# Performance work log

Measured on AMD Instinct MI355X. Metric: run time of the kernel, lower is better.

## Reference

```python
import jax, jax.numpy as jnp
import numpy as np

B, S, H, NH, T = 128, 512, 768, 8, 20
HD = H // NH


def setup_inputs() -> dict:
    key = jax.random.key(0)
    ks = jax.random.split(key, 16)
    f32 = jnp.float32
    def W(i, *shape):
        return jax.random.normal(ks[i], shape, f32) * 0.02
    inp = {}
    inp["ehs"] = jax.random.normal(ks[0], (B, S, H), f32)
    inp["relevance"] = jax.random.uniform(ks[1], (B, 1), dtype=f32)
    inp["threshold"] = jnp.array([0.5], f32)
    # text_to_caption_proj: Linear, LeakyReLU, LayerNorm, Linear
    inp["tW1"] = W(2, H, H); inp["tb1"] = jnp.zeros((H,), f32)
    inp["tg"] = jnp.ones((H,), f32); inp["tbe"] = jnp.zeros((H,), f32)
    inp["tW2"] = W(3, H, H); inp["tb2"] = jnp.zeros((H,), f32)
    # image_to_caption_proj
    inp["iW1"] = W(4, H, H); inp["ib1"] = jnp.zeros((H,), f32)
    inp["ig"] = jnp.ones((H,), f32); inp["ibe"] = jnp.zeros((H,), f32)
    inp["iW2"] = W(5, H, H); inp["ib2"] = jnp.zeros((H,), f32)
    # nn.MultiheadAttention packed in_proj [3H,H] + out_proj [H,H], x2
    inp["taWin"] = W(6, 3 * H, H); inp["taBin"] = jnp.zeros((3 * H,), f32)
    inp["taWout"] = W(7, H, H); inp["taBout"] = jnp.zeros((H,), f32)
    inp["iaWin"] = W(8, 3 * H, H); inp["iaBin"] = jnp.zeros((3 * H,), f32)
    inp["iaWout"] = W(9, H, H); inp["iaBout"] = jnp.zeros((H,), f32)
    # length_adapter: Linear, LayerNorm, ReLU
    inp["laW"] = W(10, H, H); inp["laB"] = jnp.zeros((H,), f32)
    inp["laG"] = jnp.ones((H,), f32); inp["laBe"] = jnp.zeros((H,), f32)
    # quality_estimator: Linear(H,H/2), LayerNorm, ReLU, Linear(H/2,1), Sigmoid
    inp["qW1"] = W(11, H // 2, H); inp["qB1"] = jnp.zeros((H // 2,), f32)
    inp["qG"] = jnp.ones((H // 2,), f32); inp["qBe"] = jnp.zeros((H // 2,), f32)
    inp["qW2"] = W(12, 1, H // 2); inp["qB2"] = jnp.zeros((1,), f32)
    # masks: first half = text tokens, second half = image tokens; no valid
    # image caption => torch loop gives batch_max_length=0 => target_length=20
    pos = jnp.arange(S)
    inp["sentence_mask"] = jnp.tile((pos < S // 2).astype(jnp.int32)[None], (B, 1))
    inp["image_mask"] = jnp.tile((pos >= S // 2).astype(jnp.int32)[None], (B, 1))
    inp["image_caption_mask"] = jnp.zeros((B, S), jnp.int32)
    inp["image_caption_valid"] = jnp.zeros((B,), jnp.int32)
    return inp


def _ln(x, g, b, eps=1e-5):
    m = x.mean(-1, keepdims=True)
    v = ((x - m) ** 2).mean(-1, keepdims=True)
    return (x - m) / jnp.sqrt(v + eps) * g + b


def _mha(q, k, v, Win, bIn, Wout, bOut, key_pad):
    # torch nn.MultiheadAttention, batch_first=True
    Wq, Wk, Wv = jnp.split(Win, 3, axis=0)
    bq, bk, bv = jnp.split(bIn, 3, axis=0)
    def heads(x, Wp, bp):  # [B,L,H] -> [B,NH,L,HD]
        return (x @ Wp.T + bp).reshape(x.shape[0], x.shape[1], NH, HD).transpose(0, 2, 1, 3)
    qh, kh, vh = heads(q, Wq, bq), heads(k, Wk, bk), heads(v, Wv, bv)
    scores = jnp.einsum('bhqd,bhkd->bhqk', qh, kh) / jnp.sqrt(jnp.float32(HD))
    scores = jnp.where(key_pad[:, None, None, :], -1e9, scores)
    attn = jax.nn.softmax(scores, axis=-1)
    out = jnp.einsum('bhqk,bhkd->bhqd', attn, vh)
    out = out.transpose(0, 2, 1, 3).reshape(q.shape[0], q.shape[1], H)
    return out @ Wout.T + bOut


def _sinusoid_pe():
    # vectorized replacement of the scalar double for-loop
    pos = jnp.arange(T, dtype=jnp.float32)[:, None]            # [T,1]
    i = jnp.arange(0, H, 2, dtype=jnp.float32)                 # [H/2]
    ang = pos / (10000.0 ** (i / H))                           # [T,H/2]
    pe = jnp.zeros((T, H), jnp.float32)
    pe = pe.at[:, 0::2].set(jnp.sin(ang)).at[:, 1::2].set(jnp.cos(ang))
    return pe[None]  # [1,T,H]


def reference(ehs, relevance, threshold,
              tW1, tb1, tg, tbe, tW2, tb2,
              iW1, ib1, ig, ibe, iW2, ib2,
              taWin, taBin, taWout, taBout,
              iaWin, iaBin, iaWout, iaBout,
              laW, laB, laG, laBe,
              qW1, qB1, qG, qBe, qW2, qB2,
              sentence_mask, image_mask, image_caption_mask, image_caption_valid):
    sm = sentence_mask.astype(jnp.float32)[..., None]   # [B,S,1]
    im = image_mask.astype(jnp.float32)[..., None]
    text_emb = ehs * sm
    image_emb = ehs * im
    # image_caption_valid is all False => target_length = min(20, max_length-2) = T (static)
    text_len = jnp.clip(sm.sum(axis=1), 1e-9)            # [B,1]
    img_len = jnp.clip(im.sum(axis=1), 1e-9)
    text_pooled = (text_emb * sm).sum(axis=1) / text_len  # mask applied twice, as in torch
    image_pooled = (image_emb * im).sum(axis=1) / img_len
    def proj(x, W1, b1, g, be, W2, b2):
        h = jax.nn.leaky_relu(x @ W1.T + b1, 0.01)
        return _ln(h, g, be) @ W2.T + b2
    text_seed = proj(text_pooled, tW1, tb1, tg, tbe, tW2, tb2)
    image_seed = proj(image_pooled, iW1, ib1, ig, ibe, iW2, ib2)
    alpha = relevance                                     # relevance_score provided
    caption_seed = alpha * image_seed + (1.0 - alpha) * text_seed
    query = caption_seed[:, None, :] + _sinusoid_pe()     # [B,T,H]
    text_cap = _mha(query, text_emb, text_emb, taWin, taBin, taWout, taBout, sentence_mask == 0)
    image_cap = _mha(query, image_emb, image_emb, iaWin, iaBin, iaWout, iaBout, image_mask == 0)
    beta = relevance[:, :, None]                          # [B,1,1]
    cap = beta * image_cap + (1.0 - beta) * text_cap
    cap = jax.nn.relu(_ln(cap @ laW.T + laB, laG, laBe))  # length_adapter
    m = cap.mean(axis=1)
    h = jax.nn.relu(_ln(m @ qW1.T + qB1, qG, qBe))
    quality = jax.nn.sigmoid(h @ qW2.T + qB2)             # [B,1]
    return cap, quality
```

## Files before the change

kernel.cpp:

```cpp
#include <hip/hip_runtime.h>
#include <hip/hip_bf16.h>
#include <math.h>

#define B_  128
#define S_  512
#define H_  768
#define NH_ 8
#define T_  20
#define HD_ 96

typedef unsigned short u16;
typedef unsigned int   u32;

typedef __attribute__((ext_vector_type(8))) short bhalf8;
typedef __attribute__((ext_vector_type(4))) float f32x4;

union U8 { bhalf8 s; u32 u[4]; };

__device__ __forceinline__ f32x4 mfma16(bhalf8 a, bhalf8 b, f32x4 c){
  return __builtin_amdgcn_mfma_f32_16x16x32_bf16(a, b, c, 0, 0, 0);
}
__device__ __forceinline__ u32 cvtpk(float lo, float hi){
  u32 r; asm volatile("v_cvt_pk_bf16_f32 %0, %1, %2" : "=v"(r) : "v"(lo), "v"(hi));
  return r;
}
__device__ __forceinline__ float wsum(float v){
  #pragma unroll
  for(int o=32;o;o>>=1) v += __shfl_xor(v,o);
  return v;
}
__device__ __forceinline__ u16 f2bf(float f){
  u32 u = __float_as_uint(f);
  u32 r = (u + 0x7fffu + ((u>>16)&1u)) >> 16;
  return (u16)r;
}
__device__ __forceinline__ float bf2f(u32 bits){
  return __uint_as_float(bits<<16);
}

__global__ void k_cvtall(const float* __restrict__ s0, const float* __restrict__ s1,
                         const float* __restrict__ s2, const float* __restrict__ s3,
                         const float* __restrict__ s4, const float* __restrict__ s5,
                         const float* __restrict__ s6, const float* __restrict__ s7,
                         const float* __restrict__ s8, const float* __restrict__ s9,
                         const float* __restrict__ s10, const float* __restrict__ s11,
                         u16* __restrict__ dst){
  const int NP = (H_*H_)/2;
  int idx = blockIdx.x*256 + threadIdx.x;
  int seg, po;
  if(idx < 11*NP){ seg = idx / NP; po = idx - seg*NP; }
  else           { seg = 11; po = idx - 11*NP; if(po >= NP/2) return; }
  const float* src =
    seg==0? s0 : seg==1? s1 : seg==2? s2 : seg==3? s3 : seg==4? s4 : seg==5? s5 :
    seg==6? s6 : seg==7? s7 : seg==8? s8 : seg==9? s9 : seg==10? s10 : s11;
  u32 r = cvtpk(src[2*po], src[2*po+1]);
  *(u32*)(dst + (size_t)seg*(H_*H_) + 2*po) = r;
}

__global__ __launch_bounds__(256) void k_prep(const float* __restrict__ ehs,
                                              u16* __restrict__ ehs_b,
                                              u16* __restrict__ ehsT){
  int blk = blockIdx.x;
  int b  = blk / 96;
  int r  = blk % 96;
  int sb = r / 12, hb = r % 12;
  int s0 = sb*64, h0 = hb*64;
  __shared__ float tile[64][65];
  int t = threadIdx.x;
  const float* src = ehs + ((size_t)b*S_ + s0)*H_ + h0;
  #pragma unroll
  for(int p2=0;p2<4;p2++){
    int row = p2*16 + (t>>4);
    int c4  = (t&15)*4;
    float4 v = *(const float4*)(src + (size_t)row*H_ + c4);
    tile[row][c4+0]=v.x; tile[row][c4+1]=v.y; tile[row][c4+2]=v.z; tile[row][c4+3]=v.w;
    u32 lo = cvtpk(v.x, v.y), hi2 = cvtpk(v.z, v.w);
    u32* dst = (u32*)(ehs_b + ((size_t)b*S_ + s0 + row)*H_ + h0 + c4);
    dst[0]=lo; dst[1]=hi2;
  }
  __syncthreads();
  #pragma unroll
  for(int p2=0;p2<4;p2++){
    int hr = p2*16 + (t>>4);
    int sg = (t&15)*4;
    float a0 = tile[sg+0][hr], a1 = tile[sg+1][hr];
    float a2 = tile[sg+2][hr], a3 = tile[sg+3][hr];
    u32 lo = cvtpk(a0,a1), hi2 = cvtpk(a2,a3);
    u32* dst = (u32*)(ehsT + ((size_t)b*H_ + h0 + hr)*S_ + s0 + sg);
    dst[0]=lo; dst[1]=hi2;
  }
}

__global__ void k_wkt(const float* __restrict__ taWin, const float* __restrict__ iaWin,
                      u16* __restrict__ WkT){
  int blk = blockIdx.x; int mha = blk/576; int t = blk%576;
  const float* Wk = (mha? iaWin : taWin) + (size_t)H_*H_;
  int bx = t%24, by = t/24;
  __shared__ float tile[32][33];
  int tx = threadIdx.x & 31, ty = threadIdx.x >> 5;
  for(int rr=ty; rr<32; rr+=8) tile[rr][tx] = Wk[(size_t)(by*32+rr)*H_ + bx*32+tx];
  __syncthreads();
  u16* dst = WkT + (size_t)mha*H_*H_;
  for(int rr=ty; rr<32; rr+=8) dst[(size_t)(bx*32+rr)*H_ + by*32+tx] = f2bf(tile[tx][rr]);
}

__global__ __launch_bounds__(384) void k_pool2(const u16* __restrict__ ehs_b,
                                               const int* __restrict__ sm,
                                               const int* __restrict__ im,
                                               u16* __restrict__ pt_b, u16* __restrict__ pi_b){
  int b = blockIdx.x, tid = threadIdx.x;
  __shared__ float smf[S_], imf[S_];
  __shared__ float part[2][4][96][8];
  for(int s=tid;s<S_;s+=384){ smf[s]=(float)sm[b*S_+s]; imf[s]=(float)im[b*S_+s]; }
  __syncthreads();
  int hg = tid % 96, sp = tid / 96;
  float ts[8], is[8];
  #pragma unroll
  for(int j=0;j<8;j++){ ts[j]=0.f; is[j]=0.f; }
  for(int s=sp*128; s<sp*128+128; s++){
    U8 u; u.s = *(const bhalf8*)(ehs_b + ((size_t)b*S_+s)*H_ + hg*8);
    float mt = smf[s], mi = imf[s];
    #pragma unroll
    for(int j=0;j<4;j++){
      float lo = bf2f(u.u[j]&0xffffu), hi = bf2f(u.u[j]>>16);
      ts[2*j]   += lo*mt; ts[2*j+1] += hi*mt;
      is[2*j]   += lo*mi; is[2*j+1] += hi*mi;
    }
  }
  #pragma unroll
  for(int j=0;j<8;j++){ part[0][sp][hg][j]=ts[j]; part[1][sp][hg][j]=is[j]; }
  __syncthreads();
  float tl=0.f, il=0.f;
  for(int s=0;s<S_;s++){ tl+=smf[s]; il+=imf[s]; }
  tl = fmaxf(tl, 1e-9f); il = fmaxf(il, 1e-9f);
  for(int e=tid; e<H_; e+=384){
    int hg2 = e/8, j = e%8;
    float t = part[0][0][hg2][j]+part[0][1][hg2][j]+part[0][2][hg2][j]+part[0][3][hg2][j];
    float i2= part[1][0][hg2][j]+part[1][1][hg2][j]+part[1][2][hg2][j]+part[1][3][hg2][j];
    pt_b[b*H_+e] = f2bf(t/tl);
    pi_b[b*H_+e] = f2bf(i2/il);
  }
}

__global__ __launch_bounds__(512) void k_seed2(const u16* __restrict__ pt_b,
                                               const u16* __restrict__ pi_b,
                                               const u16* __restrict__ tW1_b, const float* __restrict__ tb1,
                                               const float* __restrict__ tg,  const float* __restrict__ tbe,
                                               const u16* __restrict__ tW2_b, const float* __restrict__ tb2,
                                               const u16* __restrict__ iW1_b, const float* __restrict__ ib1,
                                               const float* __restrict__ ig,  const float* __restrict__ ibe,
                                               const u16* __restrict__ iW2_b, const float* __restrict__ ib2,
                                               float* __restrict__ st, float* __restrict__ si){
  int which = blockIdx.x >= (B_/16);
  int row0 = (blockIdx.x - which*(B_/16))*16;
  const u16* x_b  = which? pi_b  : pt_b;
  const u16* W1_b = which? iW1_b : tW1_b;
  const float* b1 = which? ib1 : tb1;
  const float* g  = which? ig  : tg;
  const float* be = which? ibe : tbe;
  const u16* W2_b = which? iW2_b : tW2_b;
  const float* b2 = which? ib2 : tb2;
  float* out      = which? si : st;
  int tid = threadIdx.x, lane = tid&63, w = tid>>6;
  __shared__ u16 ln[16][772];
  f32x4 acc[6];
  #pragma unroll
  for(int j=0;j<6;j++) acc[j] = (f32x4){0.f,0.f,0.f,0.f};
  for(int kt=0;kt<24;kt++){
    int ko = kt*32 + (lane>>4)*8;
    bhalf8 a = *(const bhalf8*)(x_b + (size_t)(row0 + (lane&15))*H_ + ko);
    bhalf8 bb[6];
    #pragma unroll
    for(int j=0;j<6;j++){
      int row = (w*6+j)*16 + (lane&15);
      bb[j] = *(const bhalf8*)(W1_b + (size_t)row*H_ + ko);
    }
    #pragma unroll
    for(int j=0;j<6;j++) acc[j] = mfma16(a, bb[j], acc[j]);
  }
  #pragma unroll
  for(int j=0;j<6;j++){
    int c = (w*6+j)*16 + (lane&15);
    float bv = b1[c];
    #pragma unroll
    for(int rr=0;rr<4;rr++){
      int r = (lane>>4)*4 + rr;
      float v = acc[j][rr] + bv;
      ln[r][c] = f2bf((v>=0.f)? v : 0.01f*v);
    }
  }
  __syncthreads();
  for(int ri=0; ri<2; ri++){
    int r = w*2 + ri;
    float v[12]; float s = 0.f;
    #pragma unroll
    for(int i=0;i<12;i++){ v[i] = bf2f(ln[r][lane + 64*i]); s += v[i]; }
    s = wsum(s);
    float mean = s/(float)H_;
    float pv = 0.f;
    #pragma unroll
    for(int i=0;i<12;i++){ float d = v[i]-mean; pv += d*d; }
    pv = wsum(pv);
    float rstd = rsqrtf(pv/(float)H_ + 1e-5f);
    #pragma unroll
    for(int i=0;i<12;i++){
      int c = lane + 64*i;
      ln[r][c] = f2bf((v[i]-mean)*rstd*g[c] + be[c]);
    }
  }
  __syncthreads();
  f32x4 o[6];
  #pragma unroll
  for(int j=0;j<6;j++) o[j] = (f32x4){0.f,0.f,0.f,0.f};
  for(int kt=0;kt<24;kt++){
    int ko = kt*32 + (lane>>4)*8;
    bhalf8 a = *(const bhalf8*)(&ln[lane&15][ko]);
    bhalf8 bb[6];
    #pragma unroll
    for(int j=0;j<6;j++){
      int row = (w*6+j)*16 + (lane&15);
      bb[j] = *(const bhalf8*)(W2_b + (size_t)row*H_ + ko);
    }
    #pragma unroll
    for(int j=0;j<6;j++) o[j] = mfma16(a, bb[j], o[j]);
  }
  #pragma unroll
  for(int j=0;j<6;j++){
    int c = (w*6+j)*16 + (lane&15);
    float bv = b2[c];
    #pragma unroll
    for(int rr=0;rr<4;rr++){
      int r = (lane>>4)*4 + rr;
      out[(size_t)(row0 + r)*H_ + c] = o[j][rr] + bv;
    }
  }
}

__global__ void k_query(const float* __restrict__ st, const float* __restrict__ si,
                        const float* __restrict__ rel, u16* __restrict__ query_b){
  int b = blockIdx.x; int tid = threadIdx.x;
  float a = rel[b];
  const float c = 9.210340371976184f/(float)H_;
  for(int t=0;t<32;t++){
    for(int h=tid;h<H_;h+=256){
      float val = 0.f;
      if(t < T_){
        float ang = (float)t * __expf(-(float)(h & ~1) * c);
        float pe  = (h&1)? __cosf(ang) : __sinf(ang);
        val = a*si[b*H_+h] + (1.f-a)*st[b*H_+h] + pe;
      }
      query_b[(size_t)b*32*H_ + t*H_ + h] = f2bf(val);
    }
  }
}

__global__ __launch_bounds__(512) void k_qh(const u16* __restrict__ query_b,
                                            const u16* __restrict__ Wq_b,
                                            const float* __restrict__ taBin,
                                            const float* __restrict__ iaBin,
                                            u16* __restrict__ qh_b){
  int gb = blockIdx.x; int b = gb>>1, mha = gb&1;
  int tid = threadIdx.x, lane = tid&63, w = tid>>6;
  const u16* Q  = query_b + (size_t)b*32*H_;
  const u16* Wq = Wq_b + (size_t)mha*H_*H_;
  const float* bIn = mha? iaBin : taBin;
  u16* out = qh_b + (size_t)gb*32*H_;
  f32x4 acc[2][6];
  #pragma unroll
  for(int i=0;i<2;i++)
    #pragma unroll
    for(int j=0;j<6;j++) acc[i][j] = (f32x4){0.f,0.f,0.f,0.f};
  for(int kt=0;kt<24;kt++){
    int ko = kt*32 + (lane>>4)*8;
    bhalf8 a[2];
    #pragma unroll
    for(int mt=0;mt<2;mt++)
      a[mt] = *(const bhalf8*)(Q + (size_t)(mt*16 + (lane&15))*H_ + ko);
    bhalf8 bb[6];
    #pragma unroll
    for(int j=0;j<6;j++){
      int row = (w*6+j)*16 + (lane&15);
      bb[j] = *(const bhalf8*)(Wq + (size_t)row*H_ + ko);
    }
    #pragma unroll
    for(int mt=0;mt<2;mt++)
      #pragma unroll
      for(int j=0;j<6;j++) acc[mt][j] = mfma16(a[mt], bb[j], acc[mt][j]);
  }
  #pragma unroll
  for(int mt=0;mt<2;mt++)
    #pragma unroll
    for(int j=0;j<6;j++){
      int col = (w*6+j)*16 + (lane&15);
      float bq = bIn[col];
      #pragma unroll
      for(int rr=0;rr<4;rr++){
        int row = mt*16 + (lane>>4)*4 + rr;
        out[(size_t)row*H_ + col] = f2bf(acc[mt][j][rr] + bq);
      }
    }
}

__global__ __launch_bounds__(512) void k_u(const u16* __restrict__ qh_b,
                                           const u16* __restrict__ WkT,
                                           const float* __restrict__ taBin,
                                           const float* __restrict__ iaBin,
                                           u16* __restrict__ U_b,
                                           float* __restrict__ bias_ws){
  int gb = blockIdx.x; int mha = gb&1;
  int tid = threadIdx.x, lane = tid&63, w = tid>>6;
  const u16* qh = qh_b + (size_t)gb*32*H_;
  const u16* Wk = WkT + (size_t)mha*H_*H_;
  u16* Up = U_b + (size_t)gb*160*H_;
  __shared__ u16 ut[20][776];
  const float rscale = 0.10206207261596577f;
  for(int h=0; h<8; h++){
    int hd0 = h*HD_;
    for(int jn=0; jn<6; jn++){
      int nb = (w*6+jn)*16 + (lane&15);
      bhalf8 bb[3];
      #pragma unroll
      for(int kt=0;kt<3;kt++)
        bb[kt] = *(const bhalf8*)(Wk + (size_t)nb*H_ + hd0 + kt*32 + (lane>>4)*8);
      #pragma unroll
      for(int mt=0; mt<2; mt++){
        bhalf8 a[3];
        #pragma unroll
        for(int kt=0;kt<3;kt++){
          int trow = mt*16 + (lane&15);
          a[kt] = *(const bhalf8*)(qh + (size_t)trow*H_ + hd0 + kt*32 + (lane>>4)*8);
        }
        f32x4 acc = (f32x4){0.f,0.f,0.f,0.f};
        #pragma unroll
        for(int kt=0;kt<3;kt++) acc = mfma16(a[kt], bb[kt], acc);
        #pragma unroll
        for(int rr=0;rr<4;rr++){
          int trow = mt*16 + (lane>>4)*4 + rr;
          if(trow < T_)
            ut[trow][nb] = f2bf(acc[rr]*rscale);
        }
      }
    }
    __syncthreads();
    for(int e=tid; e<20*384; e+=512){
      int r = e/384, c2 = (e%384)*2;
      u32 v = *(const u32*)&ut[r][c2];
      *(u32*)(Up + (size_t)(h*T_ + r)*H_ + c2) = v;
    }
    __syncthreads();
  }
  if(tid < 160){
    int h = tid/T_, t = tid%T_; int hd0 = h*HD_;
    const float* bIn = mha? iaBin : taBin;
    float p = 0.f;
    for(int d=0; d<HD_; d++)
      p += bf2f(qh[(size_t)t*H_ + hd0 + d]) * bIn[H_ + hd0 + d];
    bias_ws[gb*160 + tid] = p*rscale;
  }
}

__global__ __launch_bounds__(512,4) void k_scores2(const u16* __restrict__ ehs_b,
                                                   const u16* __restrict__ U_b,
                                                   const float* __restrict__ bias_ws,
                                                   const int* __restrict__ smask,
                                                   const int* __restrict__ imask,
                                                   u16* __restrict__ P_b){
  int g = blockIdx.x;
  int x = g & 7, sl = g >> 3;
  int b = x*16 + (sl>>2);
  int var = sl & 3; int mha = var>>1, rhalf = var&1;
  int gb = 2*b + mha;
  const int* msk = mha? imask : smask;
  int tid = threadIdx.x, lane = tid&63, w = tid>>6;
  int rbase = rhalf*80;
  __shared__ float sbias[80];
  __shared__ float pmax[80][8];
  __shared__ float psum[80][8];
  __shared__ float mfin[80], sinv[80];
  __shared__ u16 pst[16][520];
  if(tid < 80) sbias[tid] = bias_ws[gb*160 + rbase + tid];
  __syncthreads();
  const u16* Ub = U_b + (size_t)gb*160*H_;
  const u16* Eb = ehs_b + (size_t)b*S_*H_;
  bool mk[4];
  #pragma unroll
  for(int j=0;j<4;j++) mk[j] = msk[b*S_ + w*64 + j*16 + (lane&15)] != 0;

  f32x4 acc[5][4];
  #pragma unroll
  for(int i=0;i<5;i++)
    #pragma unroll
    for(int j=0;j<4;j++) acc[i][j] = (f32x4){0.f,0.f,0.f,0.f};
  for(int kt=0;kt<24;kt++){
    int ko = kt*32 + (lane>>4)*8;
    bhalf8 a[5];
    #pragma unroll
    for(int i=0;i<5;i++)
      a[i] = *(const bhalf8*)(Ub + (size_t)(rbase + i*16 + (lane&15))*H_ + ko);
    bhalf8 bb[4];
    #pragma unroll
    for(int j=0;j<4;j++)
      bb[j] = *(const bhalf8*)(Eb + (size_t)(w*64 + j*16 + (lane&15))*H_ + ko);
    #pragma unroll
    for(int i=0;i<5;i++)
      #pragma unroll
      for(int j=0;j<4;j++) acc[i][j] = mfma16(a[i], bb[j], acc[i][j]);
  }
  #pragma unroll
  for(int i=0;i<5;i++)
    #pragma unroll
    for(int rr=0;rr<4;rr++){
      int row = i*16 + (lane>>4)*4 + rr;
      float bias = sbias[row];
      float vmax = -3e38f;
      #pragma unroll
      for(int j=0;j<4;j++){
        float v = acc[i][j][rr] + bias;
        acc[i][j][rr] = v;
        if(mk[j]) vmax = fmaxf(vmax, v);
      }
      #pragma unroll
      for(int o=1;o<16;o<<=1) vmax = fmaxf(vmax, __shfl_xor(vmax,o));
      if((lane&15)==0) pmax[row][w] = vmax;
    }
  __syncthreads();
  if(tid < 80){
    float m = pmax[tid][0];
    #pragma unroll
    for(int ww=1;ww<8;ww++) m = fmaxf(m, pmax[tid][ww]);
    mfin[tid] = m;
  }
  __syncthreads();
  #pragma unroll
  for(int i=0;i<5;i++)
    #pragma unroll
    for(int rr=0;rr<4;rr++){
      int row = i*16 + (lane>>4)*4 + rr;
      float m = mfin[row];
      float ssum = 0.f;
      #pragma unroll
      for(int j=0;j<4;j++){
        float e = mk[j]? __expf(acc[i][j][rr] - m) : 0.f;
        acc[i][j][rr] = e;
        ssum += e;
      }
      #pragma unroll
      for(int o=1;o<16;o<<=1) ssum += __shfl_xor(ssum,o);
      if((lane&15)==0) psum[row][w] = ssum;
    }
  __syncthreads();
  if(tid < 80){
    float ss = 0.f;
    #pragma unroll
    for(int ww=0;ww<8;ww++) ss += psum[tid][ww];
    sinv[tid] = 1.f/ss;
  }
  __syncthreads();
  u16* Pp = P_b + (size_t)gb*160*S_ + (size_t)rbase*S_;
  for(int i=0;i<5;i++){
    #pragma unroll
    for(int rr=0;rr<4;rr++){
      int r16 = (lane>>4)*4 + rr;
      float inv = sinv[i*16 + r16];
      #pragma unroll
      for(int j=0;j<4;j++){
        int col = w*64 + j*16 + (lane&15);
        pst[r16][col] = f2bf(acc[i][j][rr]*inv);
      }
    }
    __syncthreads();
    for(int e=tid; e<16*256; e+=512){
      int r16 = e>>8, c = e&255;
      u32 v = *(const u32*)&pst[r16][2*c];
      *(u32*)(Pp + (size_t)(i*16 + r16)*S_ + 2*c) = v;
    }
    __syncthreads();
  }
}

__global__ __launch_bounds__(512) void k_ctx2(const u16* __restrict__ ehsT,
                                              const u16* __restrict__ P_b,
                                              u16* __restrict__ ctx_b){
  int g = blockIdx.x;
  int x = g & 7, sl = g >> 3;
  int b = x*16 + (sl>>2);
  int var = sl & 3; int nh = var>>1, mha = var&1;
  int tid = threadIdx.x, lane = tid&63, w = tid>>6;
  __shared__ u16 ct[80][392];
  int nbase = nh*384 + w*48;
  const u16* Pp = P_b + (size_t)(2*b+mha)*160*S_;
  f32x4 acc[10][3];
  #pragma unroll
  for(int i=0;i<10;i++)
    #pragma unroll
    for(int j=0;j<3;j++) acc[i][j] = (f32x4){0.f,0.f,0.f,0.f};
  for(int kt=0;kt<16;kt++){
    int ko = kt*32 + (lane>>4)*8;
    bhalf8 bb[3];
    #pragma unroll
    for(int t2=0;t2<3;t2++){
      int n = nbase + t2*16 + (lane&15);
      bb[t2] = *(const bhalf8*)(ehsT + ((size_t)b*H_ + n)*S_ + ko);
    }
    bhalf8 a[10];
    #pragma unroll
    for(int i=0;i<10;i++){
      int row = i*16 + (lane&15);
      a[i] = *(const bhalf8*)(Pp + (size_t)row*S_ + ko);
    }
    #pragma unroll
    for(int i=0;i<10;i++)
      #pragma unroll
      for(int t2=0;t2<3;t2++) acc[i][t2] = mfma16(a[i], bb[t2], acc[i][t2]);
  }
  u16* Cp = ctx_b + (size_t)(2*b+mha)*160*H_ + nh*384;
  #pragma unroll
  for(int half=0; half<2; half++){
    __syncthreads();
    #pragma unroll
    for(int i=0;i<5;i++)
      #pragma unroll
      for(int t2=0;t2<3;t2++)
        #pragma unroll
        for(int rr=0;rr<4;rr++){
          int rloc = i*16 + (lane>>4)*4 + rr;
          int cl = w*48 + t2*16 + (lane&15);
          ct[rloc][cl] = f2bf(acc[half*5+i][t2][rr]);
        }
    __syncthreads();
    for(int e=tid; e<80*192; e+=512){
      int r = e/192, c2 = (e%192)*2;
      u32 v = (u32)ct[r][c2] | ((u32)ct[r][c2+1]<<16);
      *(u32*)(Cp + (size_t)(half*80 + r)*H_ + c2) = v;
    }
  }
}

__global__ __launch_bounds__(512) void k_out(const u16* __restrict__ ctx_b,
                                             const u16* __restrict__ Wv_b,
                                             const u16* __restrict__ Wo_b,
                                             const float* __restrict__ taBin,
                                             const float* __restrict__ iaBin,
                                             float* __restrict__ out_t,
                                             float* __restrict__ out_i){
  int gb = blockIdx.x; int b = gb>>1, mha = gb&1;
  int tid = threadIdx.x, lane = tid&63, w = tid>>6;
  const float* bIn = mha? iaBin : taBin;
  const u16* Wv = Wv_b + (size_t)mha*H_*H_;
  const u16* Wo = Wo_b + (size_t)mha*H_*H_;
  const u16* Cp = ctx_b + (size_t)gb*160*H_;
  __shared__ u16 vt[32][784];
  int hd0 = w*HD_;
  {
    f32x4 acc[2][6];
    #pragma unroll
    for(int i=0;i<2;i++)
      #pragma unroll
      for(int j=0;j<6;j++) acc[i][j] = (f32x4){0.f,0.f,0.f,0.f};
    for(int kt=0;kt<24;kt++){
      int ko = kt*32 + (lane>>4)*8;
      bhalf8 a[2];
      #pragma unroll
      for(int mt=0;mt<2;mt++){
        int trow = mt*16 + (lane&15);
        a[mt] = *(const bhalf8*)(Cp + (size_t)(w*T_ + trow)*H_ + ko);
      }
      bhalf8 bb[6];
      #pragma unroll
      for(int j=0;j<6;j++){
        int row = hd0 + j*16 + (lane&15);
        bb[j] = *(const bhalf8*)(Wv + (size_t)row*H_ + ko);
      }
      #pragma unroll
      for(int mt=0;mt<2;mt++)
        #pragma unroll
        for(int j=0;j<6;j++) acc[mt][j] = mfma16(a[mt], bb[j], acc[mt][j]);
    }
    #pragma unroll
    for(int mt=0;mt<2;mt++)
      #pragma unroll
      for(int j=0;j<6;j++){
        int col = j*16 + (lane&15);
        float bv = bIn[2*H_ + hd0 + col];
        #pragma unroll
        for(int rr=0;rr<4;rr++){
          int trow = mt*16 + (lane>>4)*4 + rr;
          vt[trow][hd0 + col] = f2bf(acc[mt][j][rr] + bv);
        }
      }
  }
  __syncthreads();
  {
    f32x4 o[2][6];
    #pragma unroll
    for(int i=0;i<2;i++)
      #pragma unroll
      for(int j=0;j<6;j++) o[i][j] = (f32x4){0.f,0.f,0.f,0.f};
    for(int kt=0;kt<24;kt++){
      int ko = kt*32 + (lane>>4)*8;
      bhalf8 a[2];
      #pragma unroll
      for(int mt=0;mt<2;mt++)
        a[mt] = *(const bhalf8*)(&vt[mt*16 + (lane&15)][ko]);
      bhalf8 bb[6];
      #pragma unroll
      for(int j=0;j<6;j++){
        int row = (w*6+j)*16 + (lane&15);
        bb[j] = *(const bhalf8*)(Wo + (size_t)row*H_ + ko);
      }
      #pragma unroll
      for(int mt=0;mt<2;mt++)
        #pragma unroll
        for(int j=0;j<6;j++) o[mt][j] = mfma16(a[mt], bb[j], o[mt][j]);
    }
    float* op = (mha? out_i : out_t) + (size_t)b*T_*H_;
    #pragma unroll
    for(int mt=0;mt<2;mt++)
      #pragma unroll
      for(int j=0;j<6;j++){
        int col = (w*6+j)*16 + (lane&15);
        #pragma unroll
        for(int rr=0;rr<4;rr++){
          int trow = mt*16 + (lane>>4)*4 + rr;
          if(trow < T_) op[(size_t)trow*H_ + col] = o[mt][j][rr];
        }
      }
  }
}

__global__ __launch_bounds__(512) void k_cap3(const float* __restrict__ out_t,
                                              const float* __restrict__ out_i,
                                              const float* __restrict__ taBout,
                                              const float* __restrict__ iaBout,
                                              const float* __restrict__ rel,
                                              const u16* __restrict__ laW_b,
                                              const float* __restrict__ laB,
                                              const float* __restrict__ laG,
                                              const float* __restrict__ laBe,
                                              float* __restrict__ cap){
  int blk = blockIdx.x; int row0 = blk*16;
  int tid = threadIdx.x, lane = tid&63, w = tid>>6;
  __shared__ float sy[16][776];
  __shared__ float sbo[H_], sbi[H_];
  for(int j=tid;j<H_;j+=512){ sbo[j]=taBout[j]; sbi[j]=iaBout[j]; }
  __syncthreads();
  int arow = row0 + (lane&15);
  float beta = rel[arow/T_];
  f32x4 acc[6];
  #pragma unroll
  for(int j=0;j<6;j++) acc[j] = (f32x4){0.f,0.f,0.f,0.f};
  for(int kt=0;kt<24;kt++){
    int ko = kt*32 + (lane>>4)*8;
    const float* tp = out_t + (size_t)arow*H_ + ko;
    const float* ip = out_i + (size_t)arow*H_ + ko;
    float4 t0 = *(const float4*)tp, t1 = *(const float4*)(tp+4);
    float4 i0 = *(const float4*)ip, i1 = *(const float4*)(ip+4);
    float v[8];
    v[0] = beta*(i0.x+sbi[ko+0]) + (1.f-beta)*(t0.x+sbo[ko+0]);
    v[1] = beta*(i0.y+sbi[ko+1]) + (1.f-beta)*(t0.y+sbo[ko+1]);
    v[2] = beta*(i0.z+sbi[ko+2]) + (1.f-beta)*(t0.z+sbo[ko+2]);
    v[3] = beta*(i0.w+sbi[ko+3]) + (1.f-beta)*(t0.w+sbo[ko+3]);
    v[4] = beta*(i1.x+sbi[ko+4]) + (1.f-beta)*(t1.x+sbo[ko+4]);
    v[5] = beta*(i1.y+sbi[ko+5]) + (1.f-beta)*(t1.y+sbo[ko+5]);
    v[6] = beta*(i1.z+sbi[ko+6]) + (1.f-beta)*(t1.z+sbo[ko+6]);
    v[7] = beta*(i1.w+sbi[ko+7]) + (1.f-beta)*(t1.w+sbo[ko+7]);
    U8 u;
    u.u[0]=cvtpk(v[0],v[1]); u.u[1]=cvtpk(v[2],v[3]);
    u.u[2]=cvtpk(v[4],v[5]); u.u[3]=cvtpk(v[6],v[7]);
    bhalf8 a = u.s;
    bhalf8 bb[6];
    #pragma unroll
    for(int j=0;j<6;j++){
      int row = (w*6+j)*16 + (lane&15);
      bb[j] = *(const bhalf8*)(laW_b + (size_t)row*H_ + ko);
    }
    #pragma unroll
    for(int j=0;j<6;j++) acc[j] = mfma16(a, bb[j], acc[j]);
  }
  #pragma unroll
  for(int j=0;j<6;j++){
    int c = (w*6+j)*16 + (lane&15);
    float lb = laB[c];
    #pragma unroll
    for(int rr=0;rr<4;rr++){
      int r = (lane>>4)*4 + rr;
      sy[r][c] = acc[j][rr] + lb;
    }
  }
  __syncthreads();
  for(int ri=0; ri<2; ri++){
    int r = w*2 + ri;
    float v[12];
    float s = 0.f;
    #pragma unroll
    for(int i=0;i<12;i++){ v[i] = sy[r][lane + 64*i]; s += v[i]; }
    s = wsum(s);
    float mean = s/(float)H_;
    float pv = 0.f;
    #pragma unroll
    for(int i=0;i<12;i++){ float d = v[i]-mean; pv += d*d; }
    pv = wsum(pv);
    float rstd = rsqrtf(pv/(float)H_ + 1e-5f);
    float* cp = cap + (size_t)(row0 + r)*H_;
    #pragma unroll
    for(int i=0;i<12;i++){
      int c = lane + 64*i;
      float o = (v[i]-mean)*rstd*laG[c] + laBe[c];
      cp[c] = (o>0.f)? o : 0.f;
    }
  }
}

__global__ __launch_bounds__(512) void k_quality2(const float* __restrict__ cap,
                                                  const u16* __restrict__ qW1_b,
                                                  const float* __restrict__ qB1,
                                                  const float* __restrict__ qG,
                                                  const float* __restrict__ qBe,
                                                  const float* __restrict__ qW2,
                                                  const float* __restrict__ qB2,
                                                  float* __restrict__ outq){
  const int H2 = H_/2;
  int b0 = blockIdx.x*16;
  int tid = threadIdx.x, lane = tid&63, w = tid>>6;
  __shared__ u16 sm_a[16][772];
  __shared__ float sy[16][388];
  for(int e=tid; e<16*H_; e+=512){
    int r = e/H_, c = e%H_;
    const float* cp = cap + ((size_t)(b0+r)*T_)*H_ + c;
    float s = 0.f;
    #pragma unroll
    for(int t=0;t<T_;t++) s += cp[(size_t)t*H_];
    sm_a[r][c] = f2bf(s*(1.f/(float)T_));
  }
  __syncthreads();
  f32x4 acc[3];
  #pragma unroll
  for(int j=0;j<3;j++) acc[j] = (f32x4){0.f,0.f,0.f,0.f};
  for(int kt=0;kt<24;kt++){
    int ko = kt*32 + (lane>>4)*8;
    bhalf8 a = *(const bhalf8*)(&sm_a[lane&15][ko]);
    bhalf8 bb[3];
    #pragma unroll
    for(int j=0;j<3;j++){
      int row = (w*3+j)*16 + (lane&15);
      bb[j] = *(const bhalf8*)(qW1_b + (size_t)row*H_ + ko);
    }
    #pragma unroll
    for(int j=0;j<3;j++) acc[j] = mfma16(a, bb[j], acc[j]);
  }
  #pragma unroll
  for(int j=0;j<3;j++){
    int c = (w*3+j)*16 + (lane&15);
    float q1 = qB1[c];
    #pragma unroll
    for(int rr=0;rr<4;rr++){
      int r = (lane>>4)*4 + rr;
      sy[r][c] = acc[j][rr] + q1;
    }
  }
  __syncthreads();
  for(int ri=0; ri<2; ri++){
    int r = w*2 + ri;
    float v[6]; float s = 0.f;
    #pragma unroll
    for(int i=0;i<6;i++){ v[i] = sy[r][lane + 64*i]; s += v[i]; }
    s = wsum(s);
    float mean = s/(float)H2;
    float pv = 0.f;
    #pragma unroll
    for(int i=0;i<6;i++){ float d = v[i]-mean; pv += d*d; }
    pv = wsum(pv);
    float rstd = rsqrtf(pv/(float)H2 + 1e-5f);
    float dot = 0.f;
    #pragma unroll
    for(int i=0;i<6;i++){
      int c = lane + 64*i;
      float u = (v[i]-mean)*rstd*qG[c] + qBe[c];
      u = (u>0.f)? u : 0.f;
      dot += u*qW2[c];
    }
    dot = wsum(dot);
    if(lane==0){
      float z = dot + qB2[0];
      outq[b0+r] = 1.f/(1.f+__expf(-z));
    }
  }
}

extern "C" void kernel_launch(void* const* d_in, const int* in_sizes, int n_in,
                              void* d_out, int out_size, void* d_ws, size_t ws_size,
                              hipStream_t stream){
  const float* ehs    = (const float*)d_in[0];
  const float* rel    = (const float*)d_in[1];
  const float* tW1    = (const float*)d_in[3];
  const float* tb1    = (const float*)d_in[4];
  const float* tg     = (const float*)d_in[5];
  const float* tbe    = (const float*)d_in[6];
  const float* tW2    = (const float*)d_in[7];
  const float* tb2    = (const float*)d_in[8];
  const float* iW1    = (const float*)d_in[9];
  const float* ib1    = (const float*)d_in[10];
  const float* ig     = (const float*)d_in[11];
  const float* ibe    = (const float*)d_in[12];
  const float* iW2    = (const float*)d_in[13];
  const float* ib2    = (const float*)d_in[14];
  const float* taWin  = (const float*)d_in[15];
  const float* taBin  = (const float*)d_in[16];
  const float* taWout = (const float*)d_in[17];
  const float* taBout = (const float*)d_in[18];
  const float* iaWin  = (const float*)d_in[19];
  const float* iaBin  = (const float*)d_in[20];
  const float* iaWout = (const float*)d_in[21];
  const float* iaBout = (const float*)d_in[22];
  const float* laW    = (const float*)d_in[23];
  const float* laB    = (const float*)d_in[24];
  const float* laG    = (const float*)d_in[25];
  const float* laBe   = (const float*)d_in[26];
  const float* qW1    = (const float*)d_in[27];
  const float* qB1    = (const float*)d_in[28];
  const float* qG     = (const float*)d_in[29];
  const float* qBe    = (const float*)d_in[30];
  const float* qW2    = (const float*)d_in[31];
  const float* qB2    = (const float*)d_in[32];
  const int* smask    = (const int*)d_in[33];
  const int* imask    = (const int*)d_in[34];

  char* p = (char*)d_ws;
  auto take = [&](size_t bytes)->char*{
    char* r = p; p += (bytes + 255) & ~(size_t)255; return r;
  };
  float* st      = (float*)take((size_t)B_*H_*4);
  float* si      = (float*)take((size_t)B_*H_*4);
  u16*  pt_b     = (u16*)take((size_t)B_*H_*2);
  u16*  pi_b     = (u16*)take((size_t)B_*H_*2);
  u16*  query_b  = (u16*)take((size_t)B_*32*H_*2);
  u16*  qh_b     = (u16*)take((size_t)B_*2*32*H_*2);
  u16*  WkT      = (u16*)take((size_t)2*H_*H_*2);
  u16*  Wq_b     = (u16*)take((size_t)2*H_*H_*2);
  u16*  Wv_b     = (u16*)take((size_t)2*H_*H_*2);
  u16*  Wo_b     = (u16*)take((size_t)2*H_*H_*2);
  u16*  laW_b    = (u16*)take((size_t)H_*H_*2);
  u16*  tW1_b    = (u16*)take((size_t)H_*H_*2);
  u16*  tW2_b    = (u16*)take((size_t)H_*H_*2);
  u16*  iW1_b    = (u16*)take((size_t)H_*H_*2);
  u16*  iW2_b    = (u16*)take((size_t)H_*H_*2);
  u16*  qW1_b    = (u16*)take((size_t)(H_/2)*H_*2);
  float* bias_ws = (float*)take((size_t)B_*2*160*4);
  u16*  U_b      = (u16*)take((size_t)B_*2*160*H_*2);
  u16*  P_b      = (u16*)take((size_t)B_*2*160*S_*2);
  float* out_t   = (float*)take((size_t)B_*T_*H_*4);
  float* out_i   = (float*)take((size_t)B_*T_*H_*4);
  u16*  ehs_b    = (u16*)take((size_t)B_*S_*H_*2);
  u16*  ehsT     = (u16*)take((size_t)B_*H_*S_*2);
  u16*  ctx_b    = U_b;

  hipLaunchKernelGGL(k_prep, dim3(B_*96), dim3(256), 0, stream, ehs, ehs_b, ehsT);

  const int NP = (H_*H_)/2;
  const int cvtallg = (11*NP + NP/2 + 255)/256;
  hipLaunchKernelGGL(k_cvtall, dim3(cvtallg), dim3(256), 0, stream,
                     taWin, iaWin, taWin + 2*H_*H_, iaWin + 2*H_*H_,
                     taWout, iaWout, laW, tW1, tW2, iW1, iW2, qW1, Wq_b);
  hipLaunchKernelGGL(k_wkt, dim3(1152), dim3(256), 0, stream, taWin, iaWin, WkT);

  hipLaunchKernelGGL(k_pool2, dim3(B_), dim3(384), 0, stream, ehs_b, smask, imask, pt_b, pi_b);
  hipLaunchKernelGGL(k_seed2, dim3(B_/8), dim3(512), 0, stream,
                     pt_b, pi_b, tW1_b, tb1, tg, tbe, tW2_b, tb2,
                     iW1_b, ib1, ig, ibe, iW2_b, ib2, st, si);
  hipLaunchKernelGGL(k_query, dim3(B_), dim3(256), 0, stream, st, si, rel, query_b);

  hipLaunchKernelGGL(k_qh,      dim3(B_*2),  dim3(512), 0, stream, query_b, Wq_b, taBin, iaBin, qh_b);
  hipLaunchKernelGGL(k_u,       dim3(B_*2),  dim3(512), 0, stream, qh_b, WkT, taBin, iaBin, U_b, bias_ws);
  hipLaunchKernelGGL(k_scores2, dim3(B_*4),  dim3(512), 0, stream, ehs_b, U_b, bias_ws, smask, imask, P_b);
  hipLaunchKernelGGL(k_ctx2,    dim3(B_*4),  dim3(512), 0, stream, ehsT, P_b, ctx_b);
  hipLaunchKernelGGL(k_out,     dim3(B_*2),  dim3(512), 0, stream, ctx_b, Wv_b, Wo_b, taBin, iaBin, out_t, out_i);

  float* cap = (float*)d_out;
  hipLaunchKernelGGL(k_cap3, dim3((B_*T_)/16), dim3(512), 0, stream,
                     out_t, out_i, taBout, iaBout, rel, laW_b, laB, laG, laBe, cap);
  hipLaunchKernelGGL(k_quality2, dim3(B_/16), dim3(512), 0, stream,
                     cap, qW1_b, qB1, qG, qBe, qW2, qB2, cap + (size_t)B_*T_*H_);
}
```

Measured before the change: 749.0 us.

## Fuse attention scores softmax and context GEMM into one kernel

```diff
diff --git a/kernel.cpp b/kernel.cpp
--- a/kernel.cpp
+++ b/kernel.cpp
@@ -359,26 +359,27 @@
   }
 }
 
-__global__ __launch_bounds__(512,4) void k_scores2(const u16* __restrict__ ehs_b,
-                                                   const u16* __restrict__ U_b,
-                                                   const float* __restrict__ bias_ws,
-                                                   const int* __restrict__ smask,
-                                                   const int* __restrict__ imask,
-                                                   u16* __restrict__ P_b){
+__global__ __launch_bounds__(512) void k_sctx(const u16* __restrict__ ehs_b,
+                                              const u16* __restrict__ ehsT,
+                                              const u16* __restrict__ U_b,
+                                              const float* __restrict__ bias_ws,
+                                              const int* __restrict__ smask,
+                                              const int* __restrict__ imask,
+                                              u16* __restrict__ ctx_b){
   int g = blockIdx.x;
   int x = g & 7, sl = g >> 3;
-  int b = x*16 + (sl>>2);
-  int var = sl & 3; int mha = var>>1, rhalf = var&1;
+  int b = x*16 + sl/10;
+  int var = sl % 10; int mha = var/5, rblk = var%5;
   int gb = 2*b + mha;
+  int rbase = rblk*32;
   const int* msk = mha? imask : smask;
   int tid = threadIdx.x, lane = tid&63, w = tid>>6;
-  int rbase = rhalf*80;
-  __shared__ float sbias[80];
-  __shared__ float pmax[80][8];
-  __shared__ float psum[80][8];
-  __shared__ float mfin[80], sinv[80];
-  __shared__ u16 pst[16][520];
-  if(tid < 80) sbias[tid] = bias_ws[gb*160 + rbase + tid];
+  __shared__ float sbias[32];
+  __shared__ float pmax[32][8];
+  __shared__ float psum[32][8];
+  __shared__ float mfin[32], sinv[32];
+  __shared__ u16 pst[32][520];
+  if(tid < 32) sbias[tid] = bias_ws[gb*160 + rbase + tid];
   __syncthreads();
   const u16* Ub = U_b + (size_t)gb*160*H_;
   const u16* Eb = ehs_b + (size_t)b*S_*H_;
@@ -386,28 +387,28 @@
   #pragma unroll
   for(int j=0;j<4;j++) mk[j] = msk[b*S_ + w*64 + j*16 + (lane&15)] != 0;
 
-  f32x4 acc[5][4];
-  #pragma unroll
-  for(int i=0;i<5;i++)
+  f32x4 acc[2][4];
+  #pragma unroll
+  for(int i=0;i<2;i++)
     #pragma unroll
     for(int j=0;j<4;j++) acc[i][j] = (f32x4){0.f,0.f,0.f,0.f};
   for(int kt=0;kt<24;kt++){
     int ko = kt*32 + (lane>>4)*8;
-    bhalf8 a[5];
-    #pragma unroll
-    for(int i=0;i<5;i++)
+    bhalf8 a[2];
+    #pragma unroll
+    for(int i=0;i<2;i++)
       a[i] = *(const bhalf8*)(Ub + (size_t)(rbase + i*16 + (lane&15))*H_ + ko);
     bhalf8 bb[4];
     #pragma unroll
     for(int j=0;j<4;j++)
       bb[j] = *(const bhalf8*)(Eb + (size_t)(w*64 + j*16 + (lane&15))*H_ + ko);
     #pragma unroll
-    for(int i=0;i<5;i++)
+    for(int i=0;i<2;i++)
       #pragma unroll
       for(int j=0;j<4;j++) acc[i][j] = mfma16(a[i], bb[j], acc[i][j]);
   }
   #pragma unroll
-  for(int i=0;i<5;i++)
+  for(int i=0;i<2;i++)
     #pragma unroll
     for(int rr=0;rr<4;rr++){
       int row = i*16 + (lane>>4)*4 + rr;
@@ -424,7 +425,7 @@
       if((lane&15)==0) pmax[row][w] = vmax;
     }
   __syncthreads();
-  if(tid < 80){
+  if(tid < 32){
     float m = pmax[tid][0];
     #pragma unroll
     for(int ww=1;ww<8;ww++) m = fmaxf(m, pmax[tid][ww]);
@@ -432,7 +433,7 @@
   }
   __syncthreads();
   #pragma unroll
-  for(int i=0;i<5;i++)
+  for(int i=0;i<2;i++)
     #pragma unroll
     for(int rr=0;rr<4;rr++){
       int row = i*16 + (lane>>4)*4 + rr;
@@ -449,89 +450,66 @@
       if((lane&15)==0) psum[row][w] = ssum;
     }
   __syncthreads();
-  if(tid < 80){
+  if(tid < 32){
     float ss = 0.f;
     #pragma unroll
     for(int ww=0;ww<8;ww++) ss += psum[tid][ww];
     sinv[tid] = 1.f/ss;
   }
   __syncthreads();
-  u16* Pp = P_b + (size_t)gb*160*S_ + (size_t)rbase*S_;
-  for(int i=0;i<5;i++){
+  #pragma unroll
+  for(int i=0;i<2;i++)
     #pragma unroll
     for(int rr=0;rr<4;rr++){
-      int r16 = (lane>>4)*4 + rr;
-      float inv = sinv[i*16 + r16];
+      int row = i*16 + (lane>>4)*4 + rr;
+      float inv = sinv[row];
       #pragma unroll
       for(int j=0;j<4;j++){
         int col = w*64 + j*16 + (lane&15);
-        pst[r16][col] = f2bf(acc[i][j][rr]*inv);
-      }
-    }
-    __syncthreads();
-    for(int e=tid; e<16*256; e+=512){
-      int r16 = e>>8, c = e&255;
-      u32 v = *(const u32*)&pst[r16][2*c];
-      *(u32*)(Pp + (size_t)(i*16 + r16)*S_ + 2*c) = v;
-    }
-    __syncthreads();
-  }
-}
-
-__global__ __launch_bounds__(512) void k_ctx2(const u16* __restrict__ ehsT,
-                                              const u16* __restrict__ P_b,
-                                              u16* __restrict__ ctx_b){
-  int g = blockIdx.x;
-  int x = g & 7, sl = g >> 3;
-  int b = x*16 + (sl>>2);
-  int var = sl & 3; int nh = var>>1, mha = var&1;
-  int tid = threadIdx.x, lane = tid&63, w = tid>>6;
-  __shared__ u16 ct[80][392];
-  int nbase = nh*384 + w*48;
-  const u16* Pp = P_b + (size_t)(2*b+mha)*160*S_;
-  f32x4 acc[10][3];
-  #pragma unroll
-  for(int i=0;i<10;i++)
-    #pragma unroll
-    for(int j=0;j<3;j++) acc[i][j] = (f32x4){0.f,0.f,0.f,0.f};
+        pst[row][col] = f2bf(acc[i][j][rr]*inv);
+      }
+    }
+  __syncthreads();
+
+  f32x4 c2[6][2];
+  #pragma unroll
+  for(int m=0;m<6;m++)
+    #pragma unroll
+    for(int n=0;n<2;n++) c2[m][n] = (f32x4){0.f,0.f,0.f,0.f};
+  int hbase = w*96;
   for(int kt=0;kt<16;kt++){
     int ko = kt*32 + (lane>>4)*8;
-    bhalf8 bb[3];
-    #pragma unroll
-    for(int t2=0;t2<3;t2++){
-      int n = nbase + t2*16 + (lane&15);
-      bb[t2] = *(const bhalf8*)(ehsT + ((size_t)b*H_ + n)*S_ + ko);
-    }
-    bhalf8 a[10];
-    #pragma unroll
-    for(int i=0;i<10;i++){
-      int row = i*16 + (lane&15);
-      a[i] = *(const bhalf8*)(Pp + (size_t)row*S_ + ko);
-    }
-    #pragma unroll
-    for(int i=0;i<10;i++)
-      #pragma unroll
-      for(int t2=0;t2<3;t2++) acc[i][t2] = mfma16(a[i], bb[t2], acc[i][t2]);
-  }
-  u16* Cp = ctx_b + (size_t)(2*b+mha)*160*H_ + nh*384;
-  #pragma unroll
-  for(int half=0; half<2; half++){
+    bhalf8 a6[6];
+    #pragma unroll
+    for(int m=0;m<6;m++)
+      a6[m] = *(const bhalf8*)(ehsT + ((size_t)b*H_ + hbase + m*16 + (lane&15))*S_ + ko);
+    bhalf8 bp[2];
+    #pragma unroll
+    for(int n=0;n<2;n++)
+      bp[n] = *(const bhalf8*)(&pst[n*16 + (lane&15)][ko]);
+    #pragma unroll
+    for(int m=0;m<6;m++)
+      #pragma unroll
+      for(int n=0;n<2;n++) c2[m][n] = mfma16(a6[m], bp[n], c2[m][n]);
+  }
+  u16* Cp = ctx_b + (size_t)gb*160*H_ + (size_t)rbase*H_;
+  u16 (*ct)[776] = (u16(*)[776])&pst[0][0];
+  #pragma unroll
+  for(int n=0;n<2;n++){
     __syncthreads();
     #pragma unroll
-    for(int i=0;i<5;i++)
-      #pragma unroll
-      for(int t2=0;t2<3;t2++)
-        #pragma unroll
-        for(int rr=0;rr<4;rr++){
-          int rloc = i*16 + (lane>>4)*4 + rr;
-          int cl = w*48 + t2*16 + (lane&15);
-          ct[rloc][cl] = f2bf(acc[half*5+i][t2][rr]);
-        }
+    for(int m=0;m<6;m++)
+      #pragma unroll
+      for(int rr=0;rr<4;rr++){
+        int t16 = lane&15;
+        int h = hbase + m*16 + (lane>>4)*4 + rr;
+        ct[t16][h] = f2bf(c2[m][n][rr]);
+      }
     __syncthreads();
-    for(int e=tid; e<80*192; e+=512){
-      int r = e/192, c2 = (e%192)*2;
-      u32 v = (u32)ct[r][c2] | ((u32)ct[r][c2+1]<<16);
-      *(u32*)(Cp + (size_t)(half*80 + r)*H_ + c2) = v;
+    for(int e=tid; e<16*384; e+=512){
+      int r = e/384, cc = (e%384)*2;
+      u32 v = *(const u32*)&ct[r][cc];
+      *(u32*)(Cp + (size_t)(n*16 + r)*H_ + cc) = v;
     }
   }
 }
@@ -847,12 +825,11 @@
   u16*  qW1_b    = (u16*)take((size_t)(H_/2)*H_*2);
   float* bias_ws = (float*)take((size_t)B_*2*160*4);
   u16*  U_b      = (u16*)take((size_t)B_*2*160*H_*2);
-  u16*  P_b      = (u16*)take((size_t)B_*2*160*S_*2);
+  u16*  ctx_b    = (u16*)take((size_t)B_*2*160*H_*2);
   float* out_t   = (float*)take((size_t)B_*T_*H_*4);
   float* out_i   = (float*)take((size_t)B_*T_*H_*4);
   u16*  ehs_b    = (u16*)take((size_t)B_*S_*H_*2);
   u16*  ehsT     = (u16*)take((size_t)B_*H_*S_*2);
-  u16*  ctx_b    = U_b;
 
   hipLaunchKernelGGL(k_prep, dim3(B_*96), dim3(256), 0, stream, ehs, ehs_b, ehsT);
 
@@ -869,11 +846,11 @@
                      iW1_b, ib1, ig, ibe, iW2_b, ib2, st, si);
   hipLaunchKernelGGL(k_query, dim3(B_), dim3(256), 0, stream, st, si, rel, query_b);
 
-  hipLaunchKernelGGL(k_qh,      dim3(B_*2),  dim3(512), 0, stream, query_b, Wq_b, taBin, iaBin, qh_b);
-  hipLaunchKernelGGL(k_u,       dim3(B_*2),  dim3(512), 0, stream, qh_b, WkT, taBin, iaBin, U_b, bias_ws);
-  hipLaunchKernelGGL(k_scores2, dim3(B_*4),  dim3(512), 0, stream, ehs_b, U_b, bias_ws, smask, imask, P_b);
-  hipLaunchKernelGGL(k_ctx2,    dim3(B_*4),  dim3(512), 0, stream, ehsT, P_b, ctx_b);
-  hipLaunchKernelGGL(k_out,     dim3(B_*2),  dim3(512), 0, stream, ctx_b, Wv_b, Wo_b, taBin, iaBin, out_t, out_i);
+  hipLaunchKernelGGL(k_qh,    dim3(B_*2),  dim3(512), 0, stream, query_b, Wq_b, taBin, iaBin, qh_b);
+  hipLaunchKernelGGL(k_u,     dim3(B_*2),  dim3(512), 0, stream, qh_b, WkT, taBin, iaBin, U_b, bias_ws);
+  hipLaunchKernelGGL(k_sctx,  dim3(B_*10), dim3(512), 0, stream,
+                     ehs_b, ehsT, U_b, bias_ws, smask, imask, ctx_b);
+  hipLaunchKernelGGL(k_out,   dim3(B_*2),  dim3(512), 0, stream, ctx_b, Wv_b, Wo_b, taBin, iaBin, out_t, out_i);
 
   float* cap = (float*)d_out;
   hipLaunchKernelGGL(k_cap3, dim3((B_*T_)/16), dim3(512), 0, stream,
```

Result: slower. 801.7 us (+7.0%).
